# Kernel tuning notes

Measured on AMD Instinct MI355X. Metric: run time of the kernel, lower is better.

The kernel has to match this reference:

```python
import jax, jax.numpy as jnp
import numpy as np

N, DIM = 8192, 128
NEG = -1e9  # finite stand-in for -inf; exp underflows to 0 for masked entries


def setup_inputs() -> dict:
    key = jax.random.key(0)
    k1, k2, k3, k4 = jax.random.split(key, 4)
    h = jax.random.normal(k1, (N, DIM), dtype=jnp.float32)
    social_adj = jax.random.randint(k2, (N, N), 0, 2, dtype=jnp.int32)
    # nn.Linear(dim, dim, bias=False): weight [out, in]; xavier-ish scale
    W = jax.random.normal(k3, (DIM, DIM), dtype=jnp.float32) / np.sqrt(DIM)
    a = jax.random.normal(k4, (2 * DIM,), dtype=jnp.float32) / np.sqrt(2 * DIM)
    return {"h": h, "social_adj": social_adj, "W": W, "a": a}


def reference(h, social_adj, W, a):
    Wh = h @ W.T                              # [N, d]
    d = Wh.shape[1]
    a1 = Wh @ a[:d]                           # [N]
    a2 = Wh @ a[d:]                           # [N]
    e = jax.nn.leaky_relu(a1[:, None] + a2[None, :], negative_slope=0.2)  # [N, N]
    mask = social_adj != 0
    e = jnp.where(mask, e, NEG)
    alpha = jax.nn.softmax(e, axis=-1)        # [N, N]
    # rows with no neighbors: torch gives nan->0 via nan_to_num; we zero them directly
    no_neighbor = ~jnp.any(mask, axis=-1)     # [N]
    alpha = jnp.where(no_neighbor[:, None], 0.0, alpha)
    out = alpha @ Wh                          # [N, d]; already 0 on no_neighbor rows
    return out, alpha
```

## Files before the change

### kernel.cpp

```cpp
#include <hip/hip_runtime.h>
#include <hip/hip_bf16.h>

#define NN 8192
#define DIM 128
#define KS 8
#define KSL (NN / KS)
#define RPB 64
#define KC 128

typedef __attribute__((ext_vector_type(8))) short bf16x8;
typedef __attribute__((ext_vector_type(4))) float f32x4;
typedef __attribute__((ext_vector_type(4))) int i32x4;
typedef __attribute__((ext_vector_type(4))) unsigned int u32x4;
typedef __attribute__((ext_vector_type(4))) unsigned short u16x4;
typedef __attribute__((ext_vector_type(4))) short s16x4;

static __device__ inline unsigned short f2bf(float x) {
    __hip_bfloat16 b = __float2bfloat16(x);
    return *reinterpret_cast<unsigned short*>(&b);
}

struct BSplit { short hi, lo; };
static __device__ inline BSplit bsplit(float x) {
    BSplit r;
    __hip_bfloat16 h = __float2bfloat16(x);
    r.hi = *reinterpret_cast<short*>(&h);
    float rem = x - __bfloat162float(h);
    __hip_bfloat16 l = __float2bfloat16(rem);
    r.lo = *reinterpret_cast<short*>(&l);
    return r;
}

__global__ __launch_bounds__(256) void k1m(const float* __restrict__ h,
                                           const float* __restrict__ W,
                                           const float* __restrict__ a,
                                           __hip_bfloat16* __restrict__ whbT,
                                           float* __restrict__ a1g,
                                           float2* __restrict__ pk) {
    __shared__ short whi[128 * 132];
    __shared__ short wlo[128 * 132];
    __shared__ short wt[8 * 128 * 8];
    __shared__ float a_sh[256];

    const int tid = threadIdx.x;
    const int wv = tid >> 6, lane = tid & 63;
    const int r0 = blockIdx.x * 64;

    for (int idx = tid; idx < 128 * 128; idx += 256) {
        const int d = idx >> 7, k = idx & 127;
        BSplit s = bsplit(W[idx]);
        whi[d * 132 + k] = s.hi;
        wlo[d * 132 + k] = s.lo;
    }
    a_sh[tid] = a[tid];
    __syncthreads();

    f32x4 acc[8];
    #pragma unroll
    for (int n = 0; n < 8; ++n) acc[n] = (f32x4){0.f, 0.f, 0.f, 0.f};

    const int arow = r0 + wv * 16 + (lane & 15);
    const int ksub = (lane >> 4) * 8;
    const float* hp = h + (size_t)arow * DIM + ksub;

    #pragma unroll
    for (int kk = 0; kk < 128; kk += 32) {
        f32x4 x0 = *(const f32x4*)(hp + kk);
        f32x4 x1 = *(const f32x4*)(hp + kk + 4);
        bf16x8 ah, al;
        {
            BSplit s0 = bsplit(x0.x), s1 = bsplit(x0.y), s2 = bsplit(x0.z), s3 = bsplit(x0.w);
            BSplit s4 = bsplit(x1.x), s5 = bsplit(x1.y), s6 = bsplit(x1.z), s7 = bsplit(x1.w);
            ah[0] = s0.hi; al[0] = s0.lo; ah[1] = s1.hi; al[1] = s1.lo;
            ah[2] = s2.hi; al[2] = s2.lo; ah[3] = s3.hi; al[3] = s3.lo;
            ah[4] = s4.hi; al[4] = s4.lo; ah[5] = s5.hi; al[5] = s5.lo;
            ah[6] = s6.hi; al[6] = s6.lo; ah[7] = s7.hi; al[7] = s7.lo;
        }
        #pragma unroll
        for (int n = 0; n < 8; ++n) {
            const int boff = (n * 16 + (lane & 15)) * 132 + kk + ksub;
            bf16x8 bh = *(const bf16x8*)(whi + boff);
            bf16x8 bl = *(const bf16x8*)(wlo + boff);
            acc[n] = __builtin_amdgcn_mfma_f32_16x16x32_bf16(ah, bh, acc[n], 0, 0, 0);
            acc[n] = __builtin_amdgcn_mfma_f32_16x16x32_bf16(ah, bl, acc[n], 0, 0, 0);
            acc[n] = __builtin_amdgcn_mfma_f32_16x16x32_bf16(al, bh, acc[n], 0, 0, 0);
        }
    }

    float p1[4] = {0.f, 0.f, 0.f, 0.f}, p2[4] = {0.f, 0.f, 0.f, 0.f};
    #pragma unroll
    for (int n = 0; n < 8; ++n) {
        const float av1 = a_sh[n * 16 + (lane & 15)];
        const float av2 = a_sh[128 + n * 16 + (lane & 15)];
        #pragma unroll
        for (int q = 0; q < 4; ++q) {
            p1[q] += acc[n][q] * av1;
            p2[q] += acc[n][q] * av2;
        }
    }
    #pragma unroll
    for (int o = 8; o >= 1; o >>= 1) {
        #pragma unroll
        for (int q = 0; q < 4; ++q) {
            p1[q] += __shfl_xor(p1[q], o, 64);
            p2[q] += __shfl_xor(p2[q], o, 64);
        }
    }
    if ((lane & 15) == 0) {
        #pragma unroll
        for (int q = 0; q < 4; ++q) {
            const int row = r0 + wv * 16 + (lane >> 4) * 4 + q;
            a1g[row] = p1[q];
            const float E1v = expf(p2[q]);
            const float E2v = expf(0.2f * p2[q]);
            unsigned ub = (unsigned)f2bf(E1v) | ((unsigned)f2bf(E2v) << 16);
            float2 pv;
            pv.x = p2[q];
            pv.y = __uint_as_float(ub);
            pk[row] = pv;
        }
    }

    #pragma unroll
    for (int n = 0; n < 8; ++n) {
        #pragma unroll
        for (int q = 0; q < 4; ++q) {
            const int kloc = wv * 16 + (lane >> 4) * 4 + q;
            const int d = n * 16 + (lane & 15);
            wt[(kloc >> 3) * 1024 + d * 8 + (kloc & 7)] = (short)f2bf(acc[n][q]);
        }
    }
    __syncthreads();
    short* dst = reinterpret_cast<short*>(whbT) + ((size_t)r0 << 7);
    for (int idx = tid * 4; idx < 8192; idx += 1024)
        *(s16x4*)(dst + idx) = *(const s16x4*)(wt + idx);
}

__global__ __launch_bounds__(256, 8) void sa_scan(const int* __restrict__ adj,
                                                  const float* __restrict__ a1g,
                                                  const float2* __restrict__ pk,
                                                  unsigned* __restrict__ bm,
                                                  float* __restrict__ crow) {
    const int wid = threadIdx.x >> 6, lane = threadIdx.x & 63;
    const int i = blockIdx.x * 4 + wid;
    const float a1i = a1g[i];
    const int* arow = adj + (size_t)i * NN;
    unsigned* brow = bm + (size_t)i * (NN / 32);
    const float* pkf = reinterpret_cast<const float*>(pk);

    float s1 = 0.f, s2 = 0.f;
    #pragma unroll 2
    for (int it = 0; it < NN / 256; ++it) {
        const int j0 = it * 256 + lane * 4;
        i32x4 v = __builtin_nontemporal_load((const i32x4*)(arow + j0));
        unsigned long long m0 = __ballot(v.x != 0);
        unsigned long long m1 = __ballot(v.y != 0);
        unsigned long long m2 = __ballot(v.z != 0);
        unsigned long long m3 = __ballot(v.w != 0);
        if (lane == 0) {
            u32x4 w;
            w.x = (unsigned)m0; w.y = (unsigned)m1;
            w.z = (unsigned)m2; w.w = (unsigned)m3;
            *(u32x4*)(brow + it * 8) = w;
        } else if (lane == 32) {
            u32x4 w;
            w.x = (unsigned)(m0 >> 32); w.y = (unsigned)(m1 >> 32);
            w.z = (unsigned)(m2 >> 32); w.w = (unsigned)(m3 >> 32);
            *(u32x4*)(brow + it * 8 + 4) = w;
        }
        f32x4 pa = *(const f32x4*)(pkf + 2 * j0);
        f32x4 pb = *(const f32x4*)(pkf + 2 * j0 + 4);
        float x2, e1, e2; unsigned ub; bool px;

        x2 = pa.x; ub = __float_as_uint(pa.y);
        e1 = __uint_as_float(ub << 16); e2 = __uint_as_float(ub & 0xffff0000u);
        px = (a1i + x2 >= 0.f);
        s1 += (v.x && px) ? e1 : 0.f;  s2 += (v.x && !px) ? e2 : 0.f;

        x2 = pa.z; ub = __float_as_uint(pa.w);
        e1 = __uint_as_float(ub << 16); e2 = __uint_as_float(ub & 0xffff0000u);
        px = (a1i + x2 >= 0.f);
        s1 += (v.y && px) ? e1 : 0.f;  s2 += (v.y && !px) ? e2 : 0.f;

        x2 = pb.x; ub = __float_as_uint(pb.y);
        e1 = __uint_as_float(ub << 16); e2 = __uint_as_float(ub & 0xffff0000u);
        px = (a1i + x2 >= 0.f);
        s1 += (v.z && px) ? e1 : 0.f;  s2 += (v.z && !px) ? e2 : 0.f;

        x2 = pb.z; ub = __float_as_uint(pb.w);
        e1 = __uint_as_float(ub << 16); e2 = __uint_as_float(ub & 0xffff0000u);
        px = (a1i + x2 >= 0.f);
        s1 += (v.w && px) ? e1 : 0.f;  s2 += (v.w && !px) ? e2 : 0.f;
    }
    #pragma unroll
    for (int o = 32; o >= 1; o >>= 1) {
        s1 += __shfl_xor(s1, o, 64);
        s2 += __shfl_xor(s2, o, 64);
    }
    if (lane == 0) {
        float c1 = 0.f, c2 = 0.f;
        if (s1 + s2 > 0.f) {
            float e1v = expf(a1i);
            float e2v = expf(0.2f * a1i);
            float S = e1v * s1 + e2v * s2;
            c1 = e1v / S;
            c2 = e2v / S;
        }
        crow[i * 4 + 0] = c1;
        crow[i * 4 + 1] = c2;
        crow[i * 4 + 2] = a1i;
        crow[i * 4 + 3] = 0.f;
    }
}

__global__ __launch_bounds__(512, 6) void sb_pv(const unsigned* __restrict__ bm,
                                                const float* __restrict__ crowG,
                                                const float2* __restrict__ pk,
                                                const __hip_bfloat16* __restrict__ whbT,
                                                float* __restrict__ alpha,
                                                float* __restrict__ part) {
    __shared__ unsigned bmL[RPB][KSL / 32];
    __shared__ __hip_bfloat16 abuf[2][RPB][KC + 8];
    __shared__ float crowL[RPB][4];

    const int tid = threadIdx.x;
    const int wv = tid >> 6, lane = tid & 63;
    const int r0 = blockIdx.x * RPB;
    const int ks = blockIdx.y;
    const int k0 = ks * KSL;
    const float* pkf = reinterpret_cast<const float*>(pk);

    {
        const int r = tid >> 3, wq = (tid & 7) << 2;
        *(u32x4*)(&bmL[r][wq]) =
            *(const u32x4*)(bm + (size_t)(r0 + r) * (NN / 32) + ks * (KSL / 32) + wq);
        if (tid < RPB * 4)
            crowL[tid >> 2][tid & 3] = crowG[(r0 + (tid >> 2)) * 4 + (tid & 3)];
    }
    __syncthreads();

    f32x4 acc[4];
    #pragma unroll
    for (int rt = 0; rt < 4; ++rt) acc[rt] = (f32x4){0.f, 0.f, 0.f, 0.f};
    const int n0 = wv * 16;
    const short* wb = reinterpret_cast<const short*>(whbT);
    const short* bbase = wb + (size_t)(n0 + (lane & 15)) * 8 + (size_t)(lane >> 4) * 1024;

    for (int kc = 0; kc < KSL; kc += KC) {
        const int dbuf = (kc >> 7) & 1;
        #pragma unroll
        for (int v = 0; v < 4; ++v) {
            const int vid = v * 512 + tid;
            const int r = vid >> 5;
            const int c4 = (vid & 31) << 2;
            const int jl = kc + c4;
            const int j = k0 + jl;
            const int wbw = ((jl >> 8) << 3) + (((jl >> 7) & 1) << 2);
            i32x4 w4 = *(const i32x4*)(&bmL[r][wbw]);
            const unsigned p = (jl >> 2) & 31;
            const float c1 = crowL[r][0], c2 = crowL[r][1], a1i = crowL[r][2];
            f32x4 pa = *(const f32x4*)(pkf + 2 * j);
            f32x4 pb = *(const f32x4*)(pkf + 2 * j + 4);
            f32x4 al;
            {
                unsigned ub = __float_as_uint(pa.y);
                float e1 = __uint_as_float(ub << 16), e2 = __uint_as_float(ub & 0xffff0000u);
                al.x = ((w4.x >> p) & 1) ? ((a1i + pa.x >= 0.f) ? c1 * e1 : c2 * e2) : 0.f;
            }
            {
                unsigned ub = __float_as_uint(pa.w);
                float e1 = __uint_as_float(ub << 16), e2 = __uint_as_float(ub & 0xffff0000u);
                al.y = ((w4.y >> p) & 1) ? ((a1i + pa.z >= 0.f) ? c1 * e1 : c2 * e2) : 0.f;
            }
            {
                unsigned ub = __float_as_uint(pb.y);
                float e1 = __uint_as_float(ub << 16), e2 = __uint_as_float(ub & 0xffff0000u);
                al.z = ((w4.z >> p) & 1) ? ((a1i + pb.x >= 0.f) ? c1 * e1 : c2 * e2) : 0.f;
            }
            {
                unsigned ub = __float_as_uint(pb.w);
                float e1 = __uint_as_float(ub << 16), e2 = __uint_as_float(ub & 0xffff0000u);
                al.w = ((w4.w >> p) & 1) ? ((a1i + pb.z >= 0.f) ? c1 * e1 : c2 * e2) : 0.f;
            }
            __builtin_nontemporal_store(al, (f32x4*)(alpha + (size_t)(r0 + r) * NN + j));
            u16x4 ub4;
            ub4.x = f2bf(al.x); ub4.y = f2bf(al.y); ub4.z = f2bf(al.z); ub4.w = f2bf(al.w);
            *(u16x4*)(&abuf[dbuf][r][c4]) = ub4;
        }
        __syncthreads();
        #pragma unroll
        for (int kk = 0; kk < KC; kk += 32) {
            bf16x8 bf = *(const bf16x8*)(bbase + (size_t)((k0 + kc + kk) >> 3) * 1024);
            #pragma unroll
            for (int rt = 0; rt < 4; ++rt) {
                bf16x8 af = *(const bf16x8*)(&abuf[dbuf][rt * 16 + (lane & 15)][kk + 8 * (lane >> 4)]);
                acc[rt] = __builtin_amdgcn_mfma_f32_16x16x32_bf16(af, bf, acc[rt], 0, 0, 0);
            }
        }
    }

    float* pb2 = part + (size_t)ks * NN * DIM;
    const int rb = (lane >> 4) * 4;
    #pragma unroll
    for (int rt = 0; rt < 4; ++rt) {
        #pragma unroll
        for (int q = 0; q < 4; ++q)
            __builtin_nontemporal_store(acc[rt][q],
                pb2 + (size_t)(r0 + rt * 16 + rb + q) * DIM + n0 + (lane & 15));
    }
}

__global__ __launch_bounds__(256) void k5_reduce(const float* __restrict__ part,
                                                 float* __restrict__ out) {
    const size_t idx = ((size_t)blockIdx.x * 256 + threadIdx.x) * 4;
    f32x4 s = (f32x4){0.f, 0.f, 0.f, 0.f};
    #pragma unroll
    for (int ks = 0; ks < KS; ++ks)
        s += __builtin_nontemporal_load((const f32x4*)(part + (size_t)ks * NN * DIM + idx));
    *(f32x4*)(out + idx) = s;
}

extern "C" void kernel_launch(void* const* d_in, const int* in_sizes, int n_in,
                              void* d_out, int out_size, void* d_ws, size_t ws_size,
                              hipStream_t stream) {
    const float* h   = (const float*)d_in[0];
    const int*   adj = (const int*)d_in[1];
    const float* W   = (const float*)d_in[2];
    const float* a   = (const float*)d_in[3];

    float* out   = (float*)d_out;
    float* alpha = out + (size_t)NN * DIM;

    char* ws = (char*)d_ws;
    __hip_bfloat16* whbT = (__hip_bfloat16*)(ws);
    float* a1g   = (float*)(ws + 0x200000);
    float2* pk   = (float2*)(ws + 0x208000);
    float* crow  = (float*)(ws + 0x218000);
    unsigned* bm = (unsigned*)(ws + 0x240000);
    float* part  = (float*)(ws + 0xA40000);

    k1m<<<NN / 64, 256, 0, stream>>>(h, W, a, whbT, a1g, pk);
    sa_scan<<<NN / 4, 256, 0, stream>>>(adj, a1g, pk, bm, crow);
    sb_pv<<<dim3(NN / RPB, KS), 512, 0, stream>>>(bm, crow, pk, whbT, alpha, part);
    k5_reduce<<<NN * DIM / 1024, 256, 0, stream>>>(part, out);
}
```

Measured before the change: 183.5 us.

## Drop LDS staging of bitmask and row coefficients, load directly into registers

The sb_pv kernel no longer copies the adjacency bitmask and per-row softmax coefficients into shared memory behind an initial barrier. Each thread now keeps its four rows' coefficients in registers, hoists the packed column data load out of the row loop, and reads bitmask words straight from global memory. The launch-bounds occupancy hint rises from 6 to 8 blocks, and partial-sum stores and reduce loads become ordinary cached accesses so the partials can stay in cache. The trade-offs are more global bitmask loads and higher register pressure under the tighter occupancy target.

```diff
diff --git a/kernel.cpp b/kernel.cpp
--- a/kernel.cpp
+++ b/kernel.cpp
@@ -213,15 +213,13 @@
     }
 }
 
-__global__ __launch_bounds__(512, 6) void sb_pv(const unsigned* __restrict__ bm,
+__global__ __launch_bounds__(512, 8) void sb_pv(const unsigned* __restrict__ bm,
                                                 const float* __restrict__ crowG,
                                                 const float2* __restrict__ pk,
                                                 const __hip_bfloat16* __restrict__ whbT,
                                                 float* __restrict__ alpha,
                                                 float* __restrict__ part) {
-    __shared__ unsigned bmL[RPB][KSL / 32];
     __shared__ __hip_bfloat16 abuf[2][RPB][KC + 8];
-    __shared__ float crowL[RPB][4];
 
     const int tid = threadIdx.x;
     const int wv = tid >> 6, lane = tid & 63;
@@ -230,14 +228,13 @@
     const int k0 = ks * KSL;
     const float* pkf = reinterpret_cast<const float*>(pk);
 
-    {
-        const int r = tid >> 3, wq = (tid & 7) << 2;
-        *(u32x4*)(&bmL[r][wq]) =
-            *(const u32x4*)(bm + (size_t)(r0 + r) * (NN / 32) + ks * (KSL / 32) + wq);
-        if (tid < RPB * 4)
-            crowL[tid >> 2][tid & 3] = crowG[(r0 + (tid >> 2)) * 4 + (tid & 3)];
-    }
-    __syncthreads();
+    const int rloc = tid >> 5;
+    float c1r[4], c2r[4], a1r[4];
+    #pragma unroll
+    for (int v = 0; v < 4; ++v) {
+        f32x4 cw = *(const f32x4*)(crowG + (size_t)(r0 + rloc + 16 * v) * 4);
+        c1r[v] = cw.x; c2r[v] = cw.y; a1r[v] = cw.z;
+    }
 
     f32x4 acc[4];
     #pragma unroll
@@ -246,46 +243,47 @@
     const short* wb = reinterpret_cast<const short*>(whbT);
     const short* bbase = wb + (size_t)(n0 + (lane & 15)) * 8 + (size_t)(lane >> 4) * 1024;
 
+    const int cgrp = (tid & 31) << 2;
+    const unsigned pbit = tid & 31;
+
     for (int kc = 0; kc < KSL; kc += KC) {
         const int dbuf = (kc >> 7) & 1;
+        const int jl = kc + cgrp;
+        const int j = k0 + jl;
+        const int wbw = ((jl >> 8) << 3) + (((jl >> 7) & 1) << 2);
+        f32x4 pa = *(const f32x4*)(pkf + 2 * j);
+        f32x4 pb = *(const f32x4*)(pkf + 2 * j + 4);
         #pragma unroll
         for (int v = 0; v < 4; ++v) {
-            const int vid = v * 512 + tid;
-            const int r = vid >> 5;
-            const int c4 = (vid & 31) << 2;
-            const int jl = kc + c4;
-            const int j = k0 + jl;
-            const int wbw = ((jl >> 8) << 3) + (((jl >> 7) & 1) << 2);
-            i32x4 w4 = *(const i32x4*)(&bmL[r][wbw]);
-            const unsigned p = (jl >> 2) & 31;
-            const float c1 = crowL[r][0], c2 = crowL[r][1], a1i = crowL[r][2];
-            f32x4 pa = *(const f32x4*)(pkf + 2 * j);
-            f32x4 pb = *(const f32x4*)(pkf + 2 * j + 4);
+            const int r = rloc + 16 * v;
+            const int gr = r0 + r;
+            u32x4 w4 = *(const u32x4*)(bm + (size_t)gr * (NN / 32) + ks * (KSL / 32) + wbw);
+            const float c1 = c1r[v], c2 = c2r[v], a1i = a1r[v];
             f32x4 al;
             {
                 unsigned ub = __float_as_uint(pa.y);
                 float e1 = __uint_as_float(ub << 16), e2 = __uint_as_float(ub & 0xffff0000u);
-                al.x = ((w4.x >> p) & 1) ? ((a1i + pa.x >= 0.f) ? c1 * e1 : c2 * e2) : 0.f;
+                al.x = ((w4.x >> pbit) & 1) ? ((a1i + pa.x >= 0.f) ? c1 * e1 : c2 * e2) : 0.f;
             }
             {
                 unsigned ub = __float_as_uint(pa.w);
                 float e1 = __uint_as_float(ub << 16), e2 = __uint_as_float(ub & 0xffff0000u);
-                al.y = ((w4.y >> p) & 1) ? ((a1i + pa.z >= 0.f) ? c1 * e1 : c2 * e2) : 0.f;
+                al.y = ((w4.y >> pbit) & 1) ? ((a1i + pa.z >= 0.f) ? c1 * e1 : c2 * e2) : 0.f;
             }
             {
                 unsigned ub = __float_as_uint(pb.y);
                 float e1 = __uint_as_float(ub << 16), e2 = __uint_as_float(ub & 0xffff0000u);
-                al.z = ((w4.z >> p) & 1) ? ((a1i + pb.x >= 0.f) ? c1 * e1 : c2 * e2) : 0.f;
+                al.z = ((w4.z >> pbit) & 1) ? ((a1i + pb.x >= 0.f) ? c1 * e1 : c2 * e2) : 0.f;
             }
             {
                 unsigned ub = __float_as_uint(pb.w);
                 float e1 = __uint_as_float(ub << 16), e2 = __uint_as_float(ub & 0xffff0000u);
-                al.w = ((w4.w >> p) & 1) ? ((a1i + pb.z >= 0.f) ? c1 * e1 : c2 * e2) : 0.f;
-            }
-            __builtin_nontemporal_store(al, (f32x4*)(alpha + (size_t)(r0 + r) * NN + j));
+                al.w = ((w4.w >> pbit) & 1) ? ((a1i + pb.z >= 0.f) ? c1 * e1 : c2 * e2) : 0.f;
+            }
+            __builtin_nontemporal_store(al, (f32x4*)(alpha + (size_t)gr * NN + j));
             u16x4 ub4;
             ub4.x = f2bf(al.x); ub4.y = f2bf(al.y); ub4.z = f2bf(al.z); ub4.w = f2bf(al.w);
-            *(u16x4*)(&abuf[dbuf][r][c4]) = ub4;
+            *(u16x4*)(&abuf[dbuf][r][cgrp]) = ub4;
         }
         __syncthreads();
         #pragma unroll
@@ -305,8 +303,7 @@
     for (int rt = 0; rt < 4; ++rt) {
         #pragma unroll
         for (int q = 0; q < 4; ++q)
-            __builtin_nontemporal_store(acc[rt][q],
-                pb2 + (size_t)(r0 + rt * 16 + rb + q) * DIM + n0 + (lane & 15));
+            pb2[(size_t)(r0 + rt * 16 + rb + q) * DIM + n0 + (lane & 15)] = acc[rt][q];
     }
 }
 
@@ -316,7 +313,7 @@
     f32x4 s = (f32x4){0.f, 0.f, 0.f, 0.f};
     #pragma unroll
     for (int ks = 0; ks < KS; ++ks)
-        s += __builtin_nontemporal_load((const f32x4*)(part + (size_t)ks * NN * DIM + idx));
+        s += *(const f32x4*)(part + (size_t)ks * NN * DIM + idx);
     *(f32x4*)(out + idx) = s;
 }
 
```

After: 168.1 us. 1.09x faster.
